# Kernel optimization log

Hardware: AMD Instinct MI355X
Metric: run time of the kernel (lower is better)

The kernel has to match this reference:

```python
import jax, jax.numpy as jnp
import numpy as np
import math

BANDWIDTH = 0.1
_INV_SQRT_2PI = 1.0 / math.sqrt(2.0 * math.pi)


def setup_inputs() -> dict:
    key = jax.random.key(0)
    k1, k2 = jax.random.split(key)
    data = jax.random.normal(k1, (16, 32768), dtype=jnp.float32)
    c_X = jax.random.normal(k2, (256,), dtype=jnp.float32)
    return {"data": data, "dim": -1, "c_X": c_X}


def reference(data, dim, c_X):
    # data: [B, LEN] after moving `dim` to last axis; c_X: [K] grid points
    LEN = data.shape[dim]
    x = jnp.swapaxes(data, dim, -1)  # torch .transpose(dim, -1)
    inv_b = 1.0 / BANDWIDTH
    # res: [B, LEN, K] broadcasted pairwise differences
    z = (x[..., None] - c_X) * inv_b
    # standard normal pdf of z, scaled by 1/bandwidth
    pdf = (inv_b * _INV_SQRT_2PI) * jnp.exp(-0.5 * z * z)
    pdf = pdf.sum(axis=1) / LEN  # [B, K], mean over samples
    return pdf.T  # [K, B] per original permute(1, 0)
```

## Files before the change

kernel.cpp:

```cpp
#include <hip/hip_runtime.h>


constexpr int   BINS = 3072;
constexpr float H    = 0.004f;
constexpr float INVH = 250.0f;
constexpr float LO   = -6.144f;
constexpr float SFAC = 8.49321736f;
constexpr int   NT   = 1024;

__global__ __launch_bounds__(NT) void kde_fused(
    const float* __restrict__ data, const float* __restrict__ c_X,
    float* __restrict__ out, int LEN, int B) {
  __shared__ unsigned int h[BINS];
  __shared__ float red[4][256];

  const int t = threadIdx.x;
  const int b = blockIdx.x;

  uint4* h4z = (uint4*)h;
  for (int j = t; j < BINS / 4; j += NT) h4z[j] = uint4{0u, 0u, 0u, 0u};
  __syncthreads();

  const float4* src4 = (const float4*)(data + (size_t)b * LEN);
  const int iters = LEN / (4 * NT);
  for (int i = 0; i < iters; ++i) {
    float4 x = src4[i * NT + t];
    float v[4] = {x.x, x.y, x.z, x.w};
#pragma unroll
    for (int e = 0; e < 4; ++e) {
      float p = fmaf(v[e], INVH, -LO * INVH);
      p = fminf(fmaxf(p, 1.0f), (float)(BINS - 2));
      int          ib = (int)p;
      float        f  = p - (float)ib;
      unsigned int w1 = (unsigned int)(f * 32768.0f + 0.5f);
      atomicAdd(&h[ib], 32768u - w1);
      atomicAdd(&h[ib + 1], w1);
    }
  }
  __syncthreads();

  const int k = t & 255, part = t >> 8;
  const float c = c_X[k];
  int m = (int)fmaf(c, INVH, -LO * INVH + 0.5f);
  int lo4 = ((m & ~3) - 128) >> 2;
  lo4 = max(0, min(BINS / 4 - 64, lo4));

  const float dt = H * SFAC;
  float tl = (fmaf((float)(lo4 * 4 + part * 64), H, LO) - c) * SFAC;

  const uint4* h4 = (const uint4*)h;
  const int base = lo4 + part * 16;
  float acc = 0.f;
#pragma unroll 4
  for (int j4 = 0; j4 < 16; ++j4) {
    uint4 w = h4[base + j4];
    float t0 = tl, t1 = tl + dt, t2 = tl + 2.f * dt, t3 = tl + 3.f * dt;
    acc = fmaf((float)w.x, __builtin_amdgcn_exp2f(-(t0 * t0)), acc);
    acc = fmaf((float)w.y, __builtin_amdgcn_exp2f(-(t1 * t1)), acc);
    acc = fmaf((float)w.z, __builtin_amdgcn_exp2f(-(t2 * t2)), acc);
    acc = fmaf((float)w.w, __builtin_amdgcn_exp2f(-(t3 * t3)), acc);
    tl += 4.f * dt;
  }
  red[part][k] = acc;
  __syncthreads();

  if (t < 256) {
    float s = (red[0][t] + red[1][t]) + (red[2][t] + red[3][t]);
    const float norm = 3.98942280f / ((float)LEN * 32768.0f);
    out[(size_t)t * B + b] = s * norm;
  }
}

extern "C" void kernel_launch(void* const* d_in, const int* in_sizes, int n_in,
                              void* d_out, int out_size, void* d_ws, size_t ws_size,
                              hipStream_t stream) {
  const float* data = (const float*)d_in[0];
  const float* c_X  = (const float*)d_in[2];
  float* out        = (float*)d_out;

  const int B   = 16;
  const int LEN = in_sizes[0] / B;

  kde_fused<<<dim3(B), NT, 0, stream>>>(data, c_X, out, LEN, B);
}
```

Before: 64.09 us.

## Split histogram build across many blocks with workspace partials and separate eval kernel

Moves histogram construction out of a single block per batch row into a separate kernel with 16 blocks per row, each binning one segment into its own shared-memory histogram. The partial histograms are written to workspace, and a second kernel sums them and runs the Gaussian evaluation. This is meant to replace a 16-block launch that leaves most compute units idle with 256 blocks. The cost is a second launch plus workspace writes and reads of the partial histograms.

```diff
diff --git a/kernel.cpp b/kernel.cpp
--- a/kernel.cpp
+++ b/kernel.cpp
@@ -6,25 +6,24 @@
 constexpr float INVH = 250.0f;
 constexpr float LO   = -6.144f;
 constexpr float SFAC = 8.49321736f;
+constexpr int   QH   = 16;
 constexpr int   NT   = 1024;
 
-__global__ __launch_bounds__(NT) void kde_fused(
-    const float* __restrict__ data, const float* __restrict__ c_X,
-    float* __restrict__ out, int LEN, int B) {
+__global__ __launch_bounds__(256) void kde_hist(
+    const float* __restrict__ data, unsigned int* __restrict__ ws, int LEN) {
   __shared__ unsigned int h[BINS];
-  __shared__ float red[4][256];
+  const int t = threadIdx.x;
+  const int q = blockIdx.x, b = blockIdx.y;
 
-  const int t = threadIdx.x;
-  const int b = blockIdx.x;
-
-  uint4* h4z = (uint4*)h;
-  for (int j = t; j < BINS / 4; j += NT) h4z[j] = uint4{0u, 0u, 0u, 0u};
+  uint4* h4 = (uint4*)h;
+  for (int j = t; j < BINS / 4; j += 256) h4[j] = uint4{0u, 0u, 0u, 0u};
   __syncthreads();
 
-  const float4* src4 = (const float4*)(data + (size_t)b * LEN);
-  const int iters = LEN / (4 * NT);
-  for (int i = 0; i < iters; ++i) {
-    float4 x = src4[i * NT + t];
+  const int seg = LEN / QH;
+  const float4* src4 = (const float4*)(data + (size_t)b * LEN + (size_t)q * seg);
+#pragma unroll
+  for (int i = 0; i < seg / (4 * 256); ++i) {
+    float4 x = src4[i * 256 + t];
     float v[4] = {x.x, x.y, x.z, x.w};
 #pragma unroll
     for (int e = 0; e < 4; ++e) {
@@ -36,6 +35,28 @@
       atomicAdd(&h[ib], 32768u - w1);
       atomicAdd(&h[ib + 1], w1);
     }
+  }
+  __syncthreads();
+
+  uint4* o4 = (uint4*)(ws + ((size_t)b * QH + q) * BINS);
+  for (int j = t; j < BINS / 4; j += 256) o4[j] = h4[j];
+}
+
+__global__ __launch_bounds__(NT) void kde_eval(
+    const unsigned int* __restrict__ ws, const float* __restrict__ c_X,
+    float* __restrict__ out, int LEN, int B) {
+  __shared__ unsigned int h[BINS];
+  __shared__ float red[4][256];
+
+  const int t = threadIdx.x;
+  const int b = blockIdx.x;
+
+  const unsigned int* p = ws + (size_t)b * QH * BINS;
+  for (int j = t; j < BINS; j += NT) {
+    unsigned int s = 0;
+#pragma unroll
+    for (int q = 0; q < QH; ++q) s += p[q * BINS + j];
+    h[j] = s;
   }
   __syncthreads();
 
@@ -74,12 +95,14 @@
 extern "C" void kernel_launch(void* const* d_in, const int* in_sizes, int n_in,
                               void* d_out, int out_size, void* d_ws, size_t ws_size,
                               hipStream_t stream) {
-  const float* data = (const float*)d_in[0];
-  const float* c_X  = (const float*)d_in[2];
-  float* out        = (float*)d_out;
+  const float* data  = (const float*)d_in[0];
+  const float* c_X   = (const float*)d_in[2];
+  float* out         = (float*)d_out;
+  unsigned int* ws   = (unsigned int*)d_ws;
 
   const int B   = 16;
   const int LEN = in_sizes[0] / B;
 
-  kde_fused<<<dim3(B), NT, 0, stream>>>(data, c_X, out, LEN, B);
+  kde_hist<<<dim3(QH, B), 256, 0, stream>>>(data, ws, LEN);
+  kde_eval<<<dim3(B), NT, 0, stream>>>(ws, c_X, out, LEN, B);
 }
```

Measured after the change: 67.82 us. 1.06x slower.
